# Optimization experiments

Hardware: AMD Instinct MI355X
Metric: run time of the kernel (lower is better)

Reference implementation:

```python
import jax, jax.numpy as jnp
import numpy as np

LEAKY_SLOPE = 0.01  # torch nn.LeakyReLU default


def leaky_relu(x):
    return jnp.where(x >= 0, x, LEAKY_SLOPE * x)


def rgcn_conv(x, edge_index, edge_type, w_rel, w_root, b_conv):
    # PyG RGCNConv: out = x @ W_root + b + sum_r mean_{edges of rel r into i}(x_src @ W_r)
    n = x.shape[0]
    src, dst = edge_index[0], edge_index[1]
    out = x @ w_root + b_conv
    num_rel = w_rel.shape[0]
    for r in range(num_rel):  # small fixed relation count
        mask = (edge_type == r)
        msg = x[src] @ w_rel[r]                      # [E, H]
        msg = jnp.where(mask[:, None], msg, 0.0)
        agg = jax.ops.segment_sum(msg, dst, num_segments=n)          # [N, H]
        cnt = jax.ops.segment_sum(mask.astype(x.dtype), dst, num_segments=n)
        out = out + agg / jnp.maximum(cnt, 1.0)[:, None]             # mean aggr
    return out


def setup_inputs() -> dict:
    key = jax.random.key(0)
    ks = jax.random.split(key, 10)
    N, E, D_IN, H, OUT, R = 50000, 600000, 768, 128, 3, 2
    s_in = 1.0 / np.sqrt(D_IN)
    s_h = 1.0 / np.sqrt(H)
    return {
        "feature": jax.random.normal(ks[0], (N, D_IN), dtype=jnp.float32),
        "edge_index": jax.random.randint(ks[1], (2, E), 0, N, dtype=jnp.int64),
        "edge_type": jax.random.randint(ks[2], (E,), 0, R, dtype=jnp.int64),
        "w_in": jax.random.uniform(ks[3], (D_IN, H), jnp.float32, -s_in, s_in),
        "b_in": jax.random.uniform(ks[4], (H,), jnp.float32, -s_in, s_in),
        "w_rel": jax.random.uniform(ks[5], (R, H, H), jnp.float32, -s_h, s_h),
        "w_root": jax.random.uniform(ks[6], (H, H), jnp.float32, -s_h, s_h),
        "b_conv": jnp.zeros((H,), jnp.float32),
        "w_out": jax.random.uniform(ks[7], (H, OUT), jnp.float32, -s_h, s_h),
        "b_out": jax.random.uniform(ks[8], (OUT,), jnp.float32, -s_h, s_h),
    }


def reference(feature, edge_index, edge_type, w_in, b_in, w_rel, w_root, b_conv, w_out, b_out):
    x = leaky_relu(feature @ w_in + b_in)
    # NOTE: original forward applies rgcn1 twice (shared weights); dropout is
    # identity at inference; rgcn2/linear_relu_output1 are unused.
    x = rgcn_conv(x, edge_index, edge_type, w_rel, w_root, b_conv)
    x = rgcn_conv(x, edge_index, edge_type, w_rel, w_root, b_conv)
    return x @ w_out + b_out
```

## Files before the change

kernel.cpp:

```cpp
#include <hip/hip_runtime.h>

#define H 128
#define CAP 64

typedef _Float16 f16x8 __attribute__((ext_vector_type(8)));
typedef _Float16 f16x4 __attribute__((ext_vector_type(4)));
typedef float    f32x4 __attribute__((ext_vector_type(4)));

__global__ __launch_bounds__(256) void hist_fill(const int* __restrict__ src,
    const int* __restrict__ dst, const int* __restrict__ et,
    int* __restrict__ cnt, int* __restrict__ elist, int E, int N)
{
    int e = blockIdx.x * 256 + threadIdx.x;
    if (e >= E) return;
    int s = src[e], d = dst[e], t = et[e];
    int b = t * N + d;
    int pos = atomicAdd(&cnt[b], 1);
    if (pos < CAP) elist[(size_t)b * CAP + pos] = s;
}

__global__ __launch_bounds__(256) void prep_w(const float* __restrict__ w_in,
    const float* __restrict__ w_root, const float* __restrict__ w_rel,
    _Float16* __restrict__ wInT, _Float16* __restrict__ w3T, int K)
{
    int idx = blockIdx.x * 256 + threadIdx.x;
    int tot1 = K * H;
    if (idx < tot1) {
        int k = idx >> 7, c = idx & 127;
        int o = ((k >> 3) << 10) + (c << 3) + (k & 7);
        wInT[o] = (_Float16)w_in[idx];
    } else {
        int i2 = idx - tot1;
        if (i2 < 3 * H * H) {
            int m = i2 / (H * H), r2 = i2 - m * (H * H);
            int c = r2 >> 7, k = r2 & 127;
            const float* s = (m == 0) ? w_root : (w_rel + (size_t)(m - 1) * H * H);
            w3T[i2] = (_Float16)s[(size_t)k * H + c];
        }
    }
}

__global__ __launch_bounds__(256, 3) void gemm_big(const float* __restrict__ A,
    const _Float16* __restrict__ WP, const float* __restrict__ bias,
    _Float16* __restrict__ C16, int M, int K)
{
    __shared__ _Float16 As[2][8192];

    const int tid = threadIdx.x;
    const int w   = tid >> 6;
    const int l   = tid & 63;
    const int l15 = l & 15;
    const int q   = l >> 4;
    const int brow = blockIdx.x * 64;
    const int wr   = w * 16;

    const int srow = wr + (l >> 5);
    const int sk4  = (l & 31) * 4;
    const int slot = (l & 31) >> 1;
    const int half = l & 1;

    const _Float16* bp = WP + ((size_t)q * H + l15) * 8;

    float bj[8];
#pragma unroll
    for (int j = 0; j < 8; j++) bj[j] = bias[j * 16 + l15];

    f32x4 acc[8];
    const f32x4 z4 = {0.f, 0.f, 0.f, 0.f};
#pragma unroll
    for (int j = 0; j < 8; j++) acc[j] = z4;

    const int chunks = K / 128;
    float4 st[8];

    {
        const float* apc = A + sk4;
#pragma unroll
        for (int i = 0; i < 8; i++) {
            int gr = brow + srow + i * 2; if (gr >= M) gr = M - 1;
            st[i] = *(const float4*)(apc + (size_t)gr * K);
        }
#pragma unroll
        for (int i = 0; i < 8; i++) {
            int row = srow + i * 2;
            int idx = slot * 512 + ((row ^ (slot & 7)) << 3) + half * 4;
            f16x4 v; v[0] = (_Float16)st[i].x; v[1] = (_Float16)st[i].y;
                     v[2] = (_Float16)st[i].z; v[3] = (_Float16)st[i].w;
            *(f16x4*)&As[0][idx] = v;
        }
    }
    __syncthreads();

    for (int c = 0; c < chunks; c++) {
        const bool more = (c + 1) < chunks;
        if (more) {
            const float* apc = A + (c + 1) * 128 + sk4;
#pragma unroll
            for (int i = 0; i < 8; i++) {
                int gr = brow + srow + i * 2; if (gr >= M) gr = M - 1;
                st[i] = *(const float4*)(apc + (size_t)gr * K);
            }
        }
        {
            const _Float16* __restrict__ buf = As[c & 1];
#pragma unroll
            for (int ks = 0; ks < 4; ks++) {
                const int sl = ks * 4 + q;
                f16x8 af = *(const f16x8*)&buf[sl * 512 + (((wr + l15) ^ (sl & 7)) << 3)];
                const _Float16* bks = bp + (size_t)(c * 4 + ks) * 4096;
                f16x8 bf[8];
#pragma unroll
                for (int j = 0; j < 8; j++) bf[j] = *(const f16x8*)(bks + j * 128);
#pragma unroll
                for (int j = 0; j < 8; j++)
                    acc[j] = __builtin_amdgcn_mfma_f32_16x16x32_f16(af, bf[j], acc[j], 0, 0, 0);
            }
        }
        if (more) {
            _Float16* __restrict__ buf = As[(c + 1) & 1];
#pragma unroll
            for (int i = 0; i < 8; i++) {
                int row = srow + i * 2;
                int idx = slot * 512 + ((row ^ (slot & 7)) << 3) + half * 4;
                f16x4 v; v[0] = (_Float16)st[i].x; v[1] = (_Float16)st[i].y;
                         v[2] = (_Float16)st[i].z; v[3] = (_Float16)st[i].w;
                *(f16x4*)&buf[idx] = v;
            }
        }
        __syncthreads();
    }

#pragma unroll
    for (int rg = 0; rg < 4; rg++) {
        int row = brow + wr + q * 4 + rg;
        if (row < M) {
#pragma unroll
            for (int j = 0; j < 8; j++) {
                float v = acc[j][rg] + bj[j];
                v = (v >= 0.f) ? v : 0.01f * v;
                C16[(size_t)row * H + j * 16 + l15] = (_Float16)v;
            }
        }
    }
}

__global__ __launch_bounds__(512) void gemm3(const _Float16* __restrict__ X16,
    const _Float16* __restrict__ W3, const float* __restrict__ bias,
    float* __restrict__ Y, _Float16* __restrict__ Hh, int M, int mtiles,
    size_t NH)
{
    const int w   = threadIdx.x >> 6;
    const int l   = threadIdx.x & 63;
    const int l15 = l & 15;
    const int q   = l >> 4;
    const int col = w * 16 + l15;

    f16x8 bf[3][4];
#pragma unroll
    for (int m = 0; m < 3; m++) {
        const _Float16* wpp = W3 + (size_t)m * H * H + (size_t)col * H + q * 8;
#pragma unroll
        for (int c = 0; c < 4; c++) bf[m][c] = *(const f16x8*)(wpp + c * 32);
    }
    const float bj = bias[col];

    int t = blockIdx.x;
    if (t >= mtiles) return;
    f16x8 xf[4];
    {
        const _Float16* xp = X16 + ((size_t)t * 16 + l15) * H + q * 8;
#pragma unroll
        for (int c = 0; c < 4; c++) xf[c] = *(const f16x8*)(xp + c * 32);
    }

    const f32x4 z4 = {0.f, 0.f, 0.f, 0.f};
    while (true) {
        int tn = t + gridDim.x;
        bool more = tn < mtiles;
        f16x8 xnf[4];
        if (more) {
            const _Float16* xp = X16 + ((size_t)tn * 16 + l15) * H + q * 8;
#pragma unroll
            for (int c = 0; c < 4; c++) xnf[c] = *(const f16x8*)(xp + c * 32);
        }

        f32x4 a0 = z4, a1 = z4, a2 = z4;
#pragma unroll
        for (int c = 0; c < 4; c++) {
            a0 = __builtin_amdgcn_mfma_f32_16x16x32_f16(xf[c], bf[0][c], a0, 0, 0, 0);
            a1 = __builtin_amdgcn_mfma_f32_16x16x32_f16(xf[c], bf[1][c], a1, 0, 0, 0);
            a2 = __builtin_amdgcn_mfma_f32_16x16x32_f16(xf[c], bf[2][c], a2, 0, 0, 0);
        }

#pragma unroll
        for (int rg = 0; rg < 4; rg++) {
            int row = t * 16 + q * 4 + rg;
            if (row < M) {
                Y [(size_t)row * H + col]      = a0[rg] + bj;
                Hh[(size_t)row * H + col]      = (_Float16)a1[rg];
                Hh[NH + (size_t)row * H + col] = (_Float16)a2[rg];
            }
        }
        if (!more) break;
        t = tn;
#pragma unroll
        for (int c = 0; c < 4; c++) xf[c] = xnf[c];
    }
}

template<int DO_OUT>
__global__ __launch_bounds__(256) void gather_mean(const float* __restrict__ Y,
    const _Float16* __restrict__ h, const int* __restrict__ elist,
    const int* __restrict__ cnt, _Float16* __restrict__ xn, int N, size_t NH,
    const float* __restrict__ Wo, const float* __restrict__ bo,
    float* __restrict__ out)
{
    int wv = blockIdx.x * 4 + (threadIdx.x >> 6);
    int l  = threadIdx.x & 63;
    if (wv >= N) return;

    int d0r = cnt[wv], d1r = cnt[N + wv];
    int d0 = d0r < CAP ? d0r : CAP;
    int d1 = d1r < CAP ? d1r : CAP;
    float inv0 = d0r > 0 ? 1.f / (float)d0r : 0.f;
    float inv1 = d1r > 0 ? 1.f / (float)d1r : 0.f;
    const int* l0 = elist + (size_t)wv * CAP;
    const int* l1 = elist + ((size_t)N + wv) * CAP;
    const int tot = d0 + d1;

    const int eo = l >> 4;
    const int c8 = (l & 15) * 8;

    float wo0[8], wo1[8], wo2[8];
    if (DO_OUT) {
#pragma unroll
        for (int j = 0; j < 8; j++) {
            wo0[j] = Wo[(c8 + j) * 3 + 0];
            wo1[j] = Wo[(c8 + j) * 3 + 1];
            wo2[j] = Wo[(c8 + j) * 3 + 2];
        }
    }

    float acc[8];
#pragma unroll
    for (int j = 0; j < 8; j++) acc[j] = 0.f;

    const f16x8 zv = {};
    for (int p = eo; p < tot; p += 16) {
        int p1 = p + 4, p2 = p + 8, p3 = p + 12;
        bool fA = p < d0;
        int   sA  = fA ? l0[p] : l1[p - d0];
        float scA = fA ? inv0 : inv1;
        f16x8 vA  = *(const f16x8*)&h[(fA ? (size_t)0 : NH) + (size_t)sA * H + c8];
        f16x8 vB = zv, vC = zv, vD = zv;
        float scB = 0.f, scC = 0.f, scD = 0.f;
        if (p1 < tot) {
            bool f = p1 < d0;
            int s = f ? l0[p1] : l1[p1 - d0];
            scB = f ? inv0 : inv1;
            vB = *(const f16x8*)&h[(f ? (size_t)0 : NH) + (size_t)s * H + c8];
        }
        if (p2 < tot) {
            bool f = p2 < d0;
            int s = f ? l0[p2] : l1[p2 - d0];
            scC = f ? inv0 : inv1;
            vC = *(const f16x8*)&h[(f ? (size_t)0 : NH) + (size_t)s * H + c8];
        }
        if (p3 < tot) {
            bool f = p3 < d0;
            int s = f ? l0[p3] : l1[p3 - d0];
            scD = f ? inv0 : inv1;
            vD = *(const f16x8*)&h[(f ? (size_t)0 : NH) + (size_t)s * H + c8];
        }
#pragma unroll
        for (int j = 0; j < 8; j++)
            acc[j] += scA * (float)vA[j] + scB * (float)vB[j]
                    + scC * (float)vC[j] + scD * (float)vD[j];
    }

#pragma unroll
    for (int j = 0; j < 8; j++) {
        acc[j] += __shfl_xor(acc[j], 16);
        acc[j] += __shfl_xor(acc[j], 32);
    }

    float4 y0 = *(const float4*)&Y[(size_t)wv * H + c8];
    float4 y1 = *(const float4*)&Y[(size_t)wv * H + c8 + 4];
    float xv[8];
    xv[0] = acc[0] + y0.x; xv[1] = acc[1] + y0.y;
    xv[2] = acc[2] + y0.z; xv[3] = acc[3] + y0.w;
    xv[4] = acc[4] + y1.x; xv[5] = acc[5] + y1.y;
    xv[6] = acc[6] + y1.z; xv[7] = acc[7] + y1.w;

    if (DO_OUT) {
        float p0 = 0.f, p1 = 0.f, p2 = 0.f;
#pragma unroll
        for (int j = 0; j < 8; j++) {
            p0 += xv[j] * wo0[j];
            p1 += xv[j] * wo1[j];
            p2 += xv[j] * wo2[j];
        }
#pragma unroll
        for (int off = 1; off <= 8; off <<= 1) {
            p0 += __shfl_xor(p0, off);
            p1 += __shfl_xor(p1, off);
            p2 += __shfl_xor(p2, off);
        }
        if (l == 0) {
            out[(size_t)wv * 3 + 0] = p0 + bo[0];
            out[(size_t)wv * 3 + 1] = p1 + bo[1];
            out[(size_t)wv * 3 + 2] = p2 + bo[2];
        }
    } else {
        if (eo == 0) {
            f16x8 o;
#pragma unroll
            for (int j = 0; j < 8; j++) o[j] = (_Float16)xv[j];
            *(f16x8*)&xn[(size_t)wv * H + c8] = o;
        }
    }
}

__global__ __launch_bounds__(256) void out_gemm(const _Float16* __restrict__ X16,
    const float* __restrict__ Wo, const float* __restrict__ bo,
    float* __restrict__ out, int N, int OUT)
{
    int row = blockIdx.x * 4 + (threadIdx.x >> 6);
    int lane = threadIdx.x & 63;
    if (row >= N) return;
    float a0 = (float)X16[(size_t)row * H + lane];
    float a1 = (float)X16[(size_t)row * H + 64 + lane];
    for (int c = 0; c < OUT; c++) {
        float p = a0 * Wo[lane * OUT + c] + a1 * Wo[(64 + lane) * OUT + c];
        for (int off = 32; off > 0; off >>= 1) p += __shfl_down(p, off);
        if (lane == 0) out[(size_t)row * OUT + c] = p + bo[c];
    }
}

extern "C" void kernel_launch(void* const* d_in, const int* in_sizes, int n_in,
                              void* d_out, int out_size, void* d_ws, size_t ws_size,
                              hipStream_t stream) {
    const float* feature = (const float*)d_in[0];
    const int*   ei      = (const int*)d_in[1];
    const int*   et      = (const int*)d_in[2];
    const float* w_in    = (const float*)d_in[3];
    const float* b_in    = (const float*)d_in[4];
    const float* w_rel   = (const float*)d_in[5];
    const float* w_root  = (const float*)d_in[6];
    const float* b_conv  = (const float*)d_in[7];
    const float* w_out   = (const float*)d_in[8];
    const float* b_out   = (const float*)d_in[9];

    const int HH   = in_sizes[4];
    const int D_IN = in_sizes[3] / HH;
    const int N    = in_sizes[0] / D_IN;
    const int E    = in_sizes[1] / 2;
    const int R    = in_sizes[5] / (HH * HH);
    const int OUT  = in_sizes[9];

    const size_t NH = (size_t)N * H;

    char* base = (char*)d_ws;
    _Float16* wInT = (_Float16*)base;
    _Float16* w3T  = wInT + (size_t)D_IN * HH;
    _Float16* x0   = w3T + (size_t)3 * HH * HH;
    _Float16* x1   = x0 + NH;
    _Float16* h    = x1 + NH;
    float* y       = (float*)(h + (size_t)R * NH);
    int* cnt       = (int*)(y + NH);
    int* elist     = cnt + (size_t)R * N;

    hipMemsetAsync(cnt, 0, sizeof(int) * (size_t)R * N, stream);
    prep_w<<<(D_IN * HH + 3 * HH * HH + 255) / 256, 256, 0, stream>>>(
        w_in, w_root, w_rel, wInT, w3T, D_IN);
    hist_fill<<<(E + 255) / 256, 256, 0, stream>>>(ei, ei + E, et, cnt, elist, E, N);

    gemm_big<<<(N + 63) / 64, 256, 0, stream>>>(feature, wInT, b_in, x0, N, D_IN);

    const int mtiles = (N + 15) / 16;
    const int gblocks = (N + 3) / 4;

    gemm3<<<1024, 512, 0, stream>>>(x0, w3T, b_conv, y, h, N, mtiles, NH);
    gather_mean<0><<<gblocks, 256, 0, stream>>>(y, h, elist, cnt, x1, N, NH,
                                                nullptr, nullptr, nullptr);
    gemm3<<<1024, 512, 0, stream>>>(x1, w3T, b_conv, y, h, N, mtiles, NH);
    if (OUT == 3) {
        gather_mean<1><<<gblocks, 256, 0, stream>>>(y, h, elist, cnt, x0, N, NH,
                                                    w_out, b_out, (float*)d_out);
    } else {
        gather_mean<0><<<gblocks, 256, 0, stream>>>(y, h, elist, cnt, x0, N, NH,
                                                    nullptr, nullptr, nullptr);
        out_gemm<<<gblocks, 256, 0, stream>>>(x0, w_out, b_out, (float*)d_out, N, OUT);
    }
}
```

Before: 452.1 us.

## Aggregate before transform and fold final conv with output projection

Uses linearity to reorder each RGCN layer: the per-relation neighbor mean is taken over the raw 128-wide features first, then a single concatenated [x | mean0 | mean1] @ [W_root; W_rel0; W_rel1] GEMM replaces the three separate GEMM outputs. For the second layer the weights are pre-multiplied with w_out, so that layer's gather reduces directly to the 3 outputs without writing the full hidden state. This removes the fp32 Y buffer and the two fp16 per-relation message buffers, and the last gather reads one 128-wide input. In exchange it adds a concatenated 384-wide intermediate and changes the fp16 rounding points.

```diff
diff --git a/kernel.cpp b/kernel.cpp
--- a/kernel.cpp
+++ b/kernel.cpp
@@ -21,7 +21,7 @@
 
 __global__ __launch_bounds__(256) void prep_w(const float* __restrict__ w_in,
     const float* __restrict__ w_root, const float* __restrict__ w_rel,
-    _Float16* __restrict__ wInT, _Float16* __restrict__ w3T, int K)
+    _Float16* __restrict__ wInT, _Float16* __restrict__ wcatT, int K)
 {
     int idx = blockIdx.x * 256 + threadIdx.x;
     int tot1 = K * H;
@@ -31,18 +31,42 @@
         wInT[o] = (_Float16)w_in[idx];
     } else {
         int i2 = idx - tot1;
-        if (i2 < 3 * H * H) {
-            int m = i2 / (H * H), r2 = i2 - m * (H * H);
-            int c = r2 >> 7, k = r2 & 127;
-            const float* s = (m == 0) ? w_root : (w_rel + (size_t)(m - 1) * H * H);
-            w3T[i2] = (_Float16)s[(size_t)k * H + c];
-        }
+        if (i2 < H * 384) {
+            int c = i2 / 384, k = i2 - c * 384;
+            float v;
+            if (k < 128)      v = w_root[(size_t)k * H + c];
+            else if (k < 256) v = w_rel[(size_t)(k - 128) * H + c];
+            else              v = w_rel[(size_t)H * H + (size_t)(k - 256) * H + c];
+            wcatT[i2] = (_Float16)v;
+        }
+    }
+}
+
+__global__ __launch_bounds__(256) void prep_fin(const float* __restrict__ w_root,
+    const float* __restrict__ w_rel, const float* __restrict__ b_conv,
+    const float* __restrict__ w_out, const float* __restrict__ b_out,
+    float* __restrict__ wfin, float* __restrict__ bfin, int OUT)
+{
+    int idx = blockIdx.x * 256 + threadIdx.x;
+    if (idx < 3 * H) {
+        int m = idx >> 7, k = idx & 127;
+        const float* W = (m == 0) ? w_root : (w_rel + (size_t)(m - 1) * H * H);
+        for (int c = 0; c < OUT; c++) {
+            float s = 0.f;
+            for (int j = 0; j < H; j++) s += W[(size_t)k * H + j] * w_out[(size_t)j * OUT + c];
+            wfin[((size_t)m * H + k) * OUT + c] = s;
+        }
+    } else if (idx < 3 * H + OUT) {
+        int c = idx - 3 * H;
+        float s = b_out[c];
+        for (int j = 0; j < H; j++) s += b_conv[j] * w_out[(size_t)j * OUT + c];
+        bfin[c] = s;
     }
 }
 
 __global__ __launch_bounds__(256, 3) void gemm_big(const float* __restrict__ A,
     const _Float16* __restrict__ WP, const float* __restrict__ bias,
-    _Float16* __restrict__ C16, int M, int K)
+    _Float16* __restrict__ C16, int M, int K, int ldc)
 {
     __shared__ _Float16 As[2][8192];
 
@@ -138,16 +162,104 @@
             for (int j = 0; j < 8; j++) {
                 float v = acc[j][rg] + bj[j];
                 v = (v >= 0.f) ? v : 0.01f * v;
-                C16[(size_t)row * H + j * 16 + l15] = (_Float16)v;
-            }
-        }
-    }
-}
-
-__global__ __launch_bounds__(512) void gemm3(const _Float16* __restrict__ X16,
-    const _Float16* __restrict__ W3, const float* __restrict__ bias,
-    float* __restrict__ Y, _Float16* __restrict__ Hh, int M, int mtiles,
-    size_t NH)
+                C16[(size_t)row * ldc + j * 16 + l15] = (_Float16)v;
+            }
+        }
+    }
+}
+
+template<int MODE>
+__global__ __launch_bounds__(256) void gather_k(const _Float16* __restrict__ X,
+    int ldx, _Float16* __restrict__ Mout, const int* __restrict__ elist,
+    const int* __restrict__ cnt, int N,
+    const float* __restrict__ wfin, const float* __restrict__ bfin,
+    float* __restrict__ out)
+{
+    int wv = blockIdx.x * 4 + (threadIdx.x >> 6);
+    int l  = threadIdx.x & 63;
+    if (wv >= N) return;
+
+    const int eo   = l >> 4;
+    const int e2   = eo & 1;
+    const int half = l >> 5;
+    const int c8   = (l & 15) * 8;
+
+    int dr = cnt[(size_t)half * N + wv];
+    int d  = dr < CAP ? dr : CAP;
+    float inv = dr > 0 ? 1.f / (float)dr : 0.f;
+    const int* lst = elist + ((size_t)half * N + wv) * CAP;
+
+    float acc[8];
+#pragma unroll
+    for (int j = 0; j < 8; j++) acc[j] = 0.f;
+
+    const f16x8 zv = {};
+    for (int p = e2; p < d; p += 8) {
+        int p1 = p + 2, p2 = p + 4, p3 = p + 6;
+        int s0 = lst[p];
+        f16x8 v0 = *(const f16x8*)&X[(size_t)s0 * ldx + c8];
+        f16x8 v1 = zv, v2 = zv, v3 = zv;
+        if (p1 < d) { int s = lst[p1]; v1 = *(const f16x8*)&X[(size_t)s * ldx + c8]; }
+        if (p2 < d) { int s = lst[p2]; v2 = *(const f16x8*)&X[(size_t)s * ldx + c8]; }
+        if (p3 < d) { int s = lst[p3]; v3 = *(const f16x8*)&X[(size_t)s * ldx + c8]; }
+#pragma unroll
+        for (int j = 0; j < 8; j++)
+            acc[j] += (float)v0[j] + (float)v1[j] + (float)v2[j] + (float)v3[j];
+    }
+
+#pragma unroll
+    for (int j = 0; j < 8; j++) {
+        acc[j] += __shfl_xor(acc[j], 16);
+        acc[j] *= inv;
+    }
+
+    if (MODE == 0) {
+        if (eo == 0) {
+            f16x8 o;
+#pragma unroll
+            for (int j = 0; j < 8; j++) o[j] = (_Float16)acc[j];
+            *(f16x8*)&Mout[(size_t)wv * 384 + 128 + c8] = o;
+        } else if (eo == 2) {
+            f16x8 o;
+#pragma unroll
+            for (int j = 0; j < 8; j++) o[j] = (_Float16)acc[j];
+            *(f16x8*)&Mout[(size_t)wv * 384 + 256 + c8] = o;
+        }
+    } else {
+        float p0 = 0.f, p1 = 0.f, p2 = 0.f;
+        if (eo == 1) {
+            f16x8 xv = *(const f16x8*)&X[(size_t)wv * ldx + c8];
+#pragma unroll
+            for (int j = 0; j < 8; j++) {
+                float xf = (float)xv[j];
+                const float* wr = wfin + (size_t)(c8 + j) * 3;
+                p0 += xf * wr[0]; p1 += xf * wr[1]; p2 += xf * wr[2];
+            }
+        } else if (eo == 0 || eo == 2) {
+            const float* wb = wfin + (size_t)(eo == 0 ? 1 : 2) * H * 3;
+#pragma unroll
+            for (int j = 0; j < 8; j++) {
+                const float* wr = wb + (size_t)(c8 + j) * 3;
+                p0 += acc[j] * wr[0]; p1 += acc[j] * wr[1]; p2 += acc[j] * wr[2];
+            }
+        }
+#pragma unroll
+        for (int off = 1; off <= 32; off <<= 1) {
+            p0 += __shfl_xor(p0, off);
+            p1 += __shfl_xor(p1, off);
+            p2 += __shfl_xor(p2, off);
+        }
+        if (l == 0) {
+            out[(size_t)wv * 3 + 0] = p0 + bfin[0];
+            out[(size_t)wv * 3 + 1] = p1 + bfin[1];
+            out[(size_t)wv * 3 + 2] = p2 + bfin[2];
+        }
+    }
+}
+
+__global__ __launch_bounds__(512) void gemm_cat(const _Float16* __restrict__ XC,
+    const _Float16* __restrict__ WT, const float* __restrict__ bias,
+    _Float16* __restrict__ X2, int M, int mtiles, int ldc)
 {
     const int w   = threadIdx.x >> 6;
     const int l   = threadIdx.x & 63;
@@ -155,185 +267,67 @@
     const int q   = l >> 4;
     const int col = w * 16 + l15;
 
-    f16x8 bf[3][4];
-#pragma unroll
-    for (int m = 0; m < 3; m++) {
-        const _Float16* wpp = W3 + (size_t)m * H * H + (size_t)col * H + q * 8;
-#pragma unroll
-        for (int c = 0; c < 4; c++) bf[m][c] = *(const f16x8*)(wpp + c * 32);
+    f16x8 bf[12];
+    {
+        const _Float16* wpp = WT + (size_t)col * 384 + q * 8;
+#pragma unroll
+        for (int c = 0; c < 12; c++) bf[c] = *(const f16x8*)(wpp + c * 32);
     }
     const float bj = bias[col];
 
     int t = blockIdx.x;
     if (t >= mtiles) return;
-    f16x8 xf[4];
+    f16x8 xf[12];
     {
-        const _Float16* xp = X16 + ((size_t)t * 16 + l15) * H + q * 8;
-#pragma unroll
-        for (int c = 0; c < 4; c++) xf[c] = *(const f16x8*)(xp + c * 32);
+        const _Float16* xp = XC + ((size_t)t * 16 + l15) * 384 + q * 8;
+#pragma unroll
+        for (int c = 0; c < 12; c++) xf[c] = *(const f16x8*)(xp + c * 32);
     }
 
     const f32x4 z4 = {0.f, 0.f, 0.f, 0.f};
     while (true) {
         int tn = t + gridDim.x;
         bool more = tn < mtiles;
-        f16x8 xnf[4];
+        f16x8 xnf[12];
         if (more) {
-            const _Float16* xp = X16 + ((size_t)tn * 16 + l15) * H + q * 8;
-#pragma unroll
-            for (int c = 0; c < 4; c++) xnf[c] = *(const f16x8*)(xp + c * 32);
-        }
-
-        f32x4 a0 = z4, a1 = z4, a2 = z4;
-#pragma unroll
-        for (int c = 0; c < 4; c++) {
-            a0 = __builtin_amdgcn_mfma_f32_16x16x32_f16(xf[c], bf[0][c], a0, 0, 0, 0);
-            a1 = __builtin_amdgcn_mfma_f32_16x16x32_f16(xf[c], bf[1][c], a1, 0, 0, 0);
-            a2 = __builtin_amdgcn_mfma_f32_16x16x32_f16(xf[c], bf[2][c], a2, 0, 0, 0);
-        }
+            const _Float16* xp = XC + ((size_t)tn * 16 + l15) * 384 + q * 8;
+#pragma unroll
+            for (int c = 0; c < 12; c++) xnf[c] = *(const f16x8*)(xp + c * 32);
+        }
+
+        f32x4 a0 = z4;
+#pragma unroll
+        for (int c = 0; c < 12; c++)
+            a0 = __builtin_amdgcn_mfma_f32_16x16x32_f16(xf[c], bf[c], a0, 0, 0, 0);
 
 #pragma unroll
         for (int rg = 0; rg < 4; rg++) {
             int row = t * 16 + q * 4 + rg;
-            if (row < M) {
-                Y [(size_t)row * H + col]      = a0[rg] + bj;
-                Hh[(size_t)row * H + col]      = (_Float16)a1[rg];
-                Hh[NH + (size_t)row * H + col] = (_Float16)a2[rg];
-            }
+            if (row < M) X2[(size_t)row * ldc + col] = (_Float16)(a0[rg] + bj);
         }
         if (!more) break;
         t = tn;
 #pragma unroll
-        for (int c = 0; c < 4; c++) xf[c] = xnf[c];
-    }
-}
-
-template<int DO_OUT>
-__global__ __launch_bounds__(256) void gather_mean(const float* __restrict__ Y,
-    const _Float16* __restrict__ h, const int* __restrict__ elist,
-    const int* __restrict__ cnt, _Float16* __restrict__ xn, int N, size_t NH,
-    const float* __restrict__ Wo, const float* __restrict__ bo,
-    float* __restrict__ out)
-{
-    int wv = blockIdx.x * 4 + (threadIdx.x >> 6);
-    int l  = threadIdx.x & 63;
-    if (wv >= N) return;
-
-    int d0r = cnt[wv], d1r = cnt[N + wv];
-    int d0 = d0r < CAP ? d0r : CAP;
-    int d1 = d1r < CAP ? d1r : CAP;
-    float inv0 = d0r > 0 ? 1.f / (float)d0r : 0.f;
-    float inv1 = d1r > 0 ? 1.f / (float)d1r : 0.f;
-    const int* l0 = elist + (size_t)wv * CAP;
-    const int* l1 = elist + ((size_t)N + wv) * CAP;
-    const int tot = d0 + d1;
-
-    const int eo = l >> 4;
-    const int c8 = (l & 15) * 8;
-
-    float wo0[8], wo1[8], wo2[8];
-    if (DO_OUT) {
-#pragma unroll
-        for (int j = 0; j < 8; j++) {
-            wo0[j] = Wo[(c8 + j) * 3 + 0];
-            wo1[j] = Wo[(c8 + j) * 3 + 1];
-            wo2[j] = Wo[(c8 + j) * 3 + 2];
-        }
-    }
-
-    float acc[8];
-#pragma unroll
-    for (int j = 0; j < 8; j++) acc[j] = 0.f;
-
-    const f16x8 zv = {};
-    for (int p = eo; p < tot; p += 16) {
-        int p1 = p + 4, p2 = p + 8, p3 = p + 12;
-        bool fA = p < d0;
-        int   sA  = fA ? l0[p] : l1[p - d0];
-        float scA = fA ? inv0 : inv1;
-        f16x8 vA  = *(const f16x8*)&h[(fA ? (size_t)0 : NH) + (size_t)sA * H + c8];
-        f16x8 vB = zv, vC = zv, vD = zv;
-        float scB = 0.f, scC = 0.f, scD = 0.f;
-        if (p1 < tot) {
-            bool f = p1 < d0;
-            int s = f ? l0[p1] : l1[p1 - d0];
-            scB = f ? inv0 : inv1;
-            vB = *(const f16x8*)&h[(f ? (size_t)0 : NH) + (size_t)s * H + c8];
-        }
-        if (p2 < tot) {
-            bool f = p2 < d0;
-            int s = f ? l0[p2] : l1[p2 - d0];
-            scC = f ? inv0 : inv1;
-            vC = *(const f16x8*)&h[(f ? (size_t)0 : NH) + (size_t)s * H + c8];
-        }
-        if (p3 < tot) {
-            bool f = p3 < d0;
-            int s = f ? l0[p3] : l1[p3 - d0];
-            scD = f ? inv0 : inv1;
-            vD = *(const f16x8*)&h[(f ? (size_t)0 : NH) + (size_t)s * H + c8];
-        }
-#pragma unroll
-        for (int j = 0; j < 8; j++)
-            acc[j] += scA * (float)vA[j] + scB * (float)vB[j]
-                    + scC * (float)vC[j] + scD * (float)vD[j];
-    }
-
-#pragma unroll
-    for (int j = 0; j < 8; j++) {
-        acc[j] += __shfl_xor(acc[j], 16);
-        acc[j] += __shfl_xor(acc[j], 32);
-    }
-
-    float4 y0 = *(const float4*)&Y[(size_t)wv * H + c8];
-    float4 y1 = *(const float4*)&Y[(size_t)wv * H + c8 + 4];
-    float xv[8];
-    xv[0] = acc[0] + y0.x; xv[1] = acc[1] + y0.y;
-    xv[2] = acc[2] + y0.z; xv[3] = acc[3] + y0.w;
-    xv[4] = acc[4] + y1.x; xv[5] = acc[5] + y1.y;
-    xv[6] = acc[6] + y1.z; xv[7] = acc[7] + y1.w;
-
-    if (DO_OUT) {
-        float p0 = 0.f, p1 = 0.f, p2 = 0.f;
-#pragma unroll
-        for (int j = 0; j < 8; j++) {
-            p0 += xv[j] * wo0[j];
-            p1 += xv[j] * wo1[j];
-            p2 += xv[j] * wo2[j];
-        }
-#pragma unroll
-        for (int off = 1; off <= 8; off <<= 1) {
-            p0 += __shfl_xor(p0, off);
-            p1 += __shfl_xor(p1, off);
-            p2 += __shfl_xor(p2, off);
-        }
-        if (l == 0) {
-            out[(size_t)wv * 3 + 0] = p0 + bo[0];
-            out[(size_t)wv * 3 + 1] = p1 + bo[1];
-            out[(size_t)wv * 3 + 2] = p2 + bo[2];
-        }
-    } else {
-        if (eo == 0) {
-            f16x8 o;
-#pragma unroll
-            for (int j = 0; j < 8; j++) o[j] = (_Float16)xv[j];
-            *(f16x8*)&xn[(size_t)wv * H + c8] = o;
-        }
-    }
-}
-
-__global__ __launch_bounds__(256) void out_gemm(const _Float16* __restrict__ X16,
-    const float* __restrict__ Wo, const float* __restrict__ bo,
+        for (int c = 0; c < 12; c++) xf[c] = xnf[c];
+    }
+}
+
+__global__ __launch_bounds__(256) void proj_generic(const _Float16* __restrict__ XC,
+    const float* __restrict__ wfin, const float* __restrict__ bfin,
     float* __restrict__ out, int N, int OUT)
 {
     int row = blockIdx.x * 4 + (threadIdx.x >> 6);
-    int lane = threadIdx.x & 63;
+    int l = threadIdx.x & 63;
     if (row >= N) return;
-    float a0 = (float)X16[(size_t)row * H + lane];
-    float a1 = (float)X16[(size_t)row * H + 64 + lane];
+    float xv[6];
+#pragma unroll
+    for (int i = 0; i < 6; i++) xv[i] = (float)XC[(size_t)row * 384 + l * 6 + i];
     for (int c = 0; c < OUT; c++) {
-        float p = a0 * Wo[lane * OUT + c] + a1 * Wo[(64 + lane) * OUT + c];
+        float p = 0.f;
+#pragma unroll
+        for (int i = 0; i < 6; i++) p += xv[i] * wfin[(size_t)(l * 6 + i) * OUT + c];
         for (int off = 32; off > 0; off >>= 1) p += __shfl_down(p, off);
-        if (lane == 0) out[(size_t)row * OUT + c] = p + bo[c];
+        if (l == 0) out[(size_t)row * OUT + c] = p + bfin[c];
     }
 }
 
@@ -355,41 +349,40 @@
     const int D_IN = in_sizes[3] / HH;
     const int N    = in_sizes[0] / D_IN;
     const int E    = in_sizes[1] / 2;
-    const int R    = in_sizes[5] / (HH * HH);
     const int OUT  = in_sizes[9];
 
-    const size_t NH = (size_t)N * H;
-
     char* base = (char*)d_ws;
-    _Float16* wInT = (_Float16*)base;
-    _Float16* w3T  = wInT + (size_t)D_IN * HH;
-    _Float16* x0   = w3T + (size_t)3 * HH * HH;
-    _Float16* x1   = x0 + NH;
-    _Float16* h    = x1 + NH;
-    float* y       = (float*)(h + (size_t)R * NH);
-    int* cnt       = (int*)(y + NH);
-    int* elist     = cnt + (size_t)R * N;
-
-    hipMemsetAsync(cnt, 0, sizeof(int) * (size_t)R * N, stream);
-    prep_w<<<(D_IN * HH + 3 * HH * HH + 255) / 256, 256, 0, stream>>>(
-        w_in, w_root, w_rel, wInT, w3T, D_IN);
+    _Float16* wInT  = (_Float16*)base;
+    _Float16* wcatT = wInT + (size_t)D_IN * HH;
+    _Float16* xc1   = wcatT + (size_t)HH * 384;
+    _Float16* xc2   = xc1 + (size_t)N * 384;
+    float* wfin     = (float*)(xc2 + (size_t)N * 384);
+    float* bfin     = wfin + (size_t)3 * HH * (OUT > 0 ? OUT : 1);
+    int* cnt        = (int*)(bfin + ((OUT + 3) & ~3));
+    int* elist      = cnt + (size_t)2 * N;
+
+    hipMemsetAsync(cnt, 0, sizeof(int) * (size_t)2 * N, stream);
+    prep_w<<<(D_IN * HH + HH * 384 + 255) / 256, 256, 0, stream>>>(
+        w_in, w_root, w_rel, wInT, wcatT, D_IN);
+    prep_fin<<<2, 256, 0, stream>>>(w_root, w_rel, b_conv, w_out, b_out,
+                                    wfin, bfin, OUT);
     hist_fill<<<(E + 255) / 256, 256, 0, stream>>>(ei, ei + E, et, cnt, elist, E, N);
 
-    gemm_big<<<(N + 63) / 64, 256, 0, stream>>>(feature, wInT, b_in, x0, N, D_IN);
-
-    const int mtiles = (N + 15) / 16;
+    gemm_big<<<(N + 63) / 64, 256, 0, stream>>>(feature, wInT, b_in, xc1, N, D_IN, 384);
+
+    const int mtiles  = (N + 15) / 16;
     const int gblocks = (N + 3) / 4;
 
-    gemm3<<<1024, 512, 0, stream>>>(x0, w3T, b_conv, y, h, N, mtiles, NH);
-    gather_mean<0><<<gblocks, 256, 0, stream>>>(y, h, elist, cnt, x1, N, NH,
-                                                nullptr, nullptr, nullptr);
-    gemm3<<<1024, 512, 0, stream>>>(x1, w3T, b_conv, y, h, N, mtiles, NH);
+    gather_k<0><<<gblocks, 256, 0, stream>>>(xc1, 384, xc1, elist, cnt, N,
+                                             nullptr, nullptr, nullptr);
     if (OUT == 3) {
-        gather_mean<1><<<gblocks, 256, 0, stream>>>(y, h, elist, cnt, x0, N, NH,
-                                                    w_out, b_out, (float*)d_out);
+        gemm_cat<<<1024, 512, 0, stream>>>(xc1, wcatT, b_conv, xc2, N, mtiles, 128);
+        gather_k<1><<<gblocks, 256, 0, stream>>>(xc2, 128, nullptr, elist, cnt, N,
+                                                 wfin, bfin, (float*)d_out);
     } else {
-        gather_mean<0><<<gblocks, 256, 0, stream>>>(y, h, elist, cnt, x0, N, NH,
-                                                    nullptr, nullptr, nullptr);
-        out_gemm<<<gblocks, 256, 0, stream>>>(x0, w_out, b_out, (float*)d_out, N, OUT);
-    }
-}
+        gemm_cat<<<1024, 512, 0, stream>>>(xc1, wcatT, b_conv, xc2, N, mtiles, 384);
+        gather_k<0><<<gblocks, 256, 0, stream>>>(xc2, 384, xc2, elist, cnt, N,
+                                                 nullptr, nullptr, nullptr);
+        proj_generic<<<gblocks, 256, 0, stream>>>(xc2, wfin, bfin, (float*)d_out, N, OUT);
+    }
+}
```

Result: no change. 449.2 us (-0.6%).
